# Optimization experiments

Measured on AMD Instinct MI355X. Metric: run time of the kernel, lower is better.

## Reference

```python
import jax, jax.numpy as jnp
import numpy as np

NUM_GROUPS = 32
EPS = 1e-5

def group_norm(x, gamma, beta):
    # x: [B, C, L]
    B, C, L = x.shape
    g = x.reshape(B, NUM_GROUPS, C // NUM_GROUPS, L)
    mu = g.mean(axis=(2, 3), keepdims=True)
    var = g.var(axis=(2, 3), keepdims=True)
    g = (g - mu) * jax.lax.rsqrt(var + EPS)
    h = g.reshape(B, C, L)
    return h * gamma[None, :, None] + beta[None, :, None]

def conv1x1(h, W, b):
    # h: [B, C, L], W: [Cout, Cin], b: [Cout] -> [B, Cout, L]
    return jnp.einsum('oc,bcl->bol', W, h) + b[None, :, None]

def setup_inputs() -> dict:
    key = jax.random.key(0)
    ks = jax.random.split(key, 10)
    B, C, L = 8, 512, 2048
    s = 1.0 / np.sqrt(C)
    inp = {
        'x': jax.random.normal(ks[0], (B, C, L), dtype=jnp.float32),
        'gn_gamma': jnp.ones((C,), jnp.float32),
        'gn_beta': jnp.zeros((C,), jnp.float32),
        'Wq': jax.random.normal(ks[1], (C, C), jnp.float32) * s,
        'bq': jnp.zeros((C,), jnp.float32),
        'Wk': jax.random.normal(ks[2], (C, C), jnp.float32) * s,
        'bk': jnp.zeros((C,), jnp.float32),
        'Wv': jax.random.normal(ks[3], (C, C), jnp.float32) * s,
        'bv': jnp.zeros((C,), jnp.float32),
        'Wo': jax.random.normal(ks[4], (C, C), jnp.float32) * s,
        'bo': jnp.zeros((C,), jnp.float32),
    }
    return inp

def reference(x, gn_gamma, gn_beta, Wq, bq, Wk, bk, Wv, bv, Wo, bo):
    B, C, L = x.shape
    h = group_norm(x, gn_gamma, gn_beta)
    q = conv1x1(h, Wq, bq)  # [B, C, L]
    k = conv1x1(h, Wk, bk)  # [B, C, L]
    v = conv1x1(h, Wv, bv)  # [B, C, L]
    scale = 1.0 / jnp.sqrt(jnp.float32(C)).astype(x.dtype)
    w = jnp.einsum('bci,bcj->bij', q, k) * scale  # [B, L, L]
    w = jax.nn.softmax(w, axis=-1)
    a = jnp.einsum('bij,bcj->bci', w, v)  # [B, C, L]
    return x + conv1x1(a, Wo, bo)
```

## Files before the change

### kernel.cpp

```cpp
#include <hip/hip_runtime.h>
#include <hip/hip_bf16.h>

#define B_ 8
#define C_ 512
#define L_ 2048
#define G_ 32

typedef __attribute__((ext_vector_type(8))) short bf16x8;
typedef __attribute__((ext_vector_type(4))) float f32x4;

__device__ __forceinline__ float b2f(short h) {
    union { unsigned u; float f; } c; c.u = ((unsigned)(unsigned short)h) << 16; return c.f;
}
__device__ __forceinline__ short f2b(float f) {
    union { float f; unsigned u; } c; c.f = f;
    unsigned r = (c.u + 0x7FFFu + ((c.u >> 16) & 1u)) >> 16;
    return (short)r;
}

__device__ __forceinline__ void load_lds16(const void* g, void* s) {
    __builtin_amdgcn_global_load_lds(
        (const __attribute__((address_space(1))) void*)g,
        (__attribute__((address_space(3))) void*)s, 16, 0, 0);
}

__global__ __launch_bounds__(256) void zero_f32(float* __restrict__ p) {
    p[(size_t)blockIdx.x * 256 + threadIdx.x] = 0.f;
}

__global__ __launch_bounds__(256) void cvt_w(
    const float* __restrict__ a, const float* __restrict__ b,
    const float* __restrict__ c, const float* __restrict__ d,
    short* __restrict__ o)
{
    const float* src = (blockIdx.y == 0) ? a : (blockIdx.y == 1) ? b
                     : (blockIdx.y == 2) ? c : d;
    short* dst = o + (size_t)blockIdx.y * (C_ * C_);
    int i = (blockIdx.x * 256 + threadIdx.x) * 4;
    float4 v = *(const float4*)(src + i);
    short4 r;
    r.x = f2b(v.x); r.y = f2b(v.y); r.z = f2b(v.z); r.w = f2b(v.w);
    *(short4*)(dst + i) = r;
}

__global__ __launch_bounds__(256) void groupnorm_tr(
    const float* __restrict__ x, const float* __restrict__ gamma,
    const float* __restrict__ beta, short* __restrict__ h_t)
{
    int bg = blockIdx.x;
    int b = bg >> 5, g = bg & 31;
    const float* xg = x + ((size_t)b * C_ + (size_t)g * 16) * L_;
    int t = threadIdx.x;
    float s = 0.f, ss = 0.f;
    for (int i = t; i < 8192; i += 256) {
        float4 v = ((const float4*)xg)[i];
        s  += v.x + v.y + v.z + v.w;
        ss += v.x * v.x + v.y * v.y + v.z * v.z + v.w * v.w;
    }
    #pragma unroll
    for (int o = 32; o > 0; o >>= 1) { s += __shfl_down(s, o); ss += __shfl_down(ss, o); }
    __shared__ float rs[4], rss[4], stats[2], gam[16], bet[16];
    int wave = t >> 6, lane = t & 63;
    if (lane == 0) { rs[wave] = s; rss[wave] = ss; }
    if (t < 16) { gam[t] = gamma[g * 16 + t]; bet[t] = beta[g * 16 + t]; }
    __syncthreads();
    if (t == 0) {
        float S = rs[0] + rs[1] + rs[2] + rs[3];
        float SS = rss[0] + rss[1] + rss[2] + rss[3];
        float mean = S * (1.f / 32768.f);
        float var = SS * (1.f / 32768.f) - mean * mean;
        stats[0] = mean; stats[1] = rsqrtf(var + 1e-5f);
    }
    __syncthreads();
    float mean = stats[0], rstd = stats[1];
    short* ho = h_t + (size_t)b * L_ * C_ + (size_t)g * 16;
    for (int i = t; i < 32768; i += 256) {
        int cl = i & 15, l = i >> 4;
        float xv = xg[cl * L_ + l];
        float hv = (xv - mean) * rstd * gam[cl] + bet[cl];
        ho[(size_t)l * C_ + cl] = f2b(hv);
    }
}

template<int BM, int BIAS_MODE, bool RESID, bool OUTF32, bool EXPSUM, bool ROWDIV>
__global__ __launch_bounds__(BM * 2) void gemm_bt(
    const short* __restrict__ A, const short* __restrict__ Bt,
    void* __restrict__ Co, const float* __restrict__ bias,
    const float* __restrict__ bias2, const float* __restrict__ resid,
    float* __restrict__ rowsum,
    int N, int K, int lda, int ldb, int ldc,
    long sA, long sB, long sC, float alpha)
{
    constexpr int T = BM * 2;
    constexpr int RPP = T / 8;
    __shared__ __align__(16) short As[BM * 64];
    __shared__ __align__(16) short Bs[128 * 64];

    int nbx = gridDim.x, nby = gridDim.y, nbz = gridDim.z;
    int lin = blockIdx.x + nbx * (blockIdx.y + nby * blockIdx.z);
    int total = nbx * nby * nbz;
    int bx, by, bz;
    if ((total & 7) == 0) {
        int chunk = total >> 3;
        int logical = (lin & 7) * chunk + (lin >> 3);
        bx = logical % nbx; int t2 = logical / nbx; by = t2 % nby; bz = t2 / nby;
    } else { bx = blockIdx.x; by = blockIdx.y; bz = blockIdx.z; }

    const short* Ab = A + (size_t)bz * sA;
    const short* Bb = Bt + (size_t)bz * sB;
    int m0 = by * BM, n0 = bx * 128;
    int t = threadIdx.x, lane = t & 63;
    int wave = t >> 6;
    int wm = wave >> 1, wn = wave & 1;

    f32x4 acc[4][4] = {};

    int rs_ = t >> 3, cs_ = t & 7;
    int gcol = ((cs_ ^ (rs_ & 7)) << 3);
    const short* gA = Ab + (size_t)(m0 + rs_) * lda + gcol;
    const short* gB = Bb + (size_t)(n0 + rs_) * ldb + gcol;
    int fr = lane & 15, fq = lane >> 4;
    int ch0 = (fq ^ (fr & 7)) << 3;
    int ch1 = ((4 | fq) ^ (fr & 7)) << 3;

    for (int k0 = 0; k0 < K; k0 += 64) {
        __syncthreads();
        #pragma unroll
        for (int i = 0; i < BM / RPP; i++)
            load_lds16(gA + (size_t)(RPP * i) * lda, As + i * (RPP * 64) + t * 8);
        #pragma unroll
        for (int i = 0; i < 128 / RPP; i++)
            load_lds16(gB + (size_t)(RPP * i) * ldb, Bs + i * (RPP * 64) + t * 8);
        gA += 64; gB += 64;
        __syncthreads();
        #pragma unroll
        for (int kk = 0; kk < 2; kk++) {
            int ch = kk ? ch1 : ch0;
            bf16x8 af[4], bfr[4];
            #pragma unroll
            for (int i = 0; i < 4; i++) {
                int R = wm * 64 + i * 16 + fr;
                af[i] = *(const bf16x8*)(As + R * 64 + ch);
            }
            #pragma unroll
            for (int j = 0; j < 4; j++) {
                int R = wn * 64 + j * 16 + fr;
                bfr[j] = *(const bf16x8*)(Bs + R * 64 + ch);
            }
            #pragma unroll
            for (int mt = 0; mt < 4; mt++)
                #pragma unroll
                for (int nt = 0; nt < 4; nt++)
                    acc[mt][nt] = __builtin_amdgcn_mfma_f32_16x16x32_bf16(
                        af[mt], bfr[nt], acc[mt][nt], 0, 0, 0);
        }
    }

    size_t cb = (size_t)bz * sC;
    int crow = (lane >> 4) * 4;
    int wrow = wm * 64;
    float psum[4][4];
    float inv[4][4];
    if (EXPSUM) {
        #pragma unroll
        for (int mt = 0; mt < 4; mt++)
            #pragma unroll
            for (int r = 0; r < 4; r++) psum[mt][r] = 0.f;
    }
    if (ROWDIV) {
        #pragma unroll
        for (int mt = 0; mt < 4; mt++)
            #pragma unroll
            for (int r = 0; r < 4; r++) {
                int m = m0 + wrow + mt * 16 + crow + r;
                inv[mt][r] = 1.f / rowsum[(size_t)bz * L_ + m];
            }
    }
    #pragma unroll
    for (int mt = 0; mt < 4; mt++) {
        #pragma unroll
        for (int nt = 0; nt < 4; nt++) {
            int n = n0 + wn * 64 + nt * 16 + fr;
            float bn = 0.f;
            if (BIAS_MODE == 3) bn = (n < 512) ? bias[n] : bias2[n - 512];
            #pragma unroll
            for (int r = 0; r < 4; r++) {
                int m = m0 + wrow + mt * 16 + crow + r;
                float v = acc[mt][nt][r] * alpha;
                if (EXPSUM) { v = __expf(v); psum[mt][r] += v; }
                if (ROWDIV) v *= inv[mt][r];
                if (BIAS_MODE == 3) v += bn;
                if (BIAS_MODE == 2) v += bias[m];
                size_t idx = cb + (size_t)m * ldc + n;
                if (RESID) v += resid[idx];
                if (OUTF32) ((float*)Co)[idx] = v;
                else        ((short*)Co)[idx] = f2b(v);
            }
        }
    }
    if (EXPSUM) {
        #pragma unroll
        for (int mt = 0; mt < 4; mt++)
            #pragma unroll
            for (int r = 0; r < 4; r++) {
                float s = psum[mt][r];
                s += __shfl_xor(s, 1); s += __shfl_xor(s, 2);
                s += __shfl_xor(s, 4); s += __shfl_xor(s, 8);
                if ((lane & 15) == 0) {
                    int m = m0 + wrow + mt * 16 + crow + r;
                    atomicAdd(rowsum + (size_t)bz * L_ + m, s);
                }
            }
    }
}

extern "C" void kernel_launch(void* const* d_in, const int* in_sizes, int n_in,
                              void* d_out, int out_size, void* d_ws, size_t ws_size,
                              hipStream_t stream)
{
    const float* x     = (const float*)d_in[0];
    const float* gamma = (const float*)d_in[1];
    const float* beta  = (const float*)d_in[2];
    const float* Wq    = (const float*)d_in[3];
    const float* bq    = (const float*)d_in[4];
    const float* Wk    = (const float*)d_in[5];
    const float* bk    = (const float*)d_in[6];
    const float* Wv    = (const float*)d_in[7];
    const float* bv    = (const float*)d_in[8];
    const float* Wo    = (const float*)d_in[9];
    const float* bo    = (const float*)d_in[10];
    float* out = (float*)d_out;

    const size_t MiB = 1024 * 1024;
    const size_t CC = (size_t)C_ * C_;
    const size_t LC = (size_t)L_ * C_;
    const size_t LL = (size_t)L_ * L_;
    const size_t wbytes = 4 * CC * sizeof(short);

    const size_t perb = 16 * MiB + L_ * sizeof(float);
    int nb = 1;
    for (int c = 8; c >= 1; c >>= 1)
        if (ws_size >= wbytes + (size_t)c * perb) { nb = c; break; }

    short* wq_b = (short*)d_ws;
    short* wv_b = wq_b + 2 * CC;
    short* wo_b = wv_b + CC;
    short* h_t  = wo_b + CC;
    short* qk_t = h_t + (size_t)nb * LC;
    short* v_   = qk_t + (size_t)nb * 2 * LC;
    short* S    = v_  + (size_t)nb * LC;
    float* rsum = (float*)(S + (size_t)nb * LL);
    short* a_t  = h_t;

    const long sLC = (long)LC;
    const long sLL = (long)LL;
    const float scale = 0.044194173824159216f;

    cvt_w<<<dim3(C_ * C_ / 1024, 4), 256, 0, stream>>>(Wq, Wk, Wv, Wo, wq_b);

    for (int b0 = 0; b0 < B_; b0 += nb) {
        const float* xb = x + (size_t)b0 * LC;
        float* outb = out + (size_t)b0 * LC;

        zero_f32<<<dim3(nb * L_ / 256), 256, 0, stream>>>(rsum);
        groupnorm_tr<<<dim3(nb * G_), 256, 0, stream>>>(xb, gamma, beta, h_t);

        gemm_bt<128, 3, false, false, false, false><<<dim3(8, 16, nb), 256, 0, stream>>>(
            h_t, wq_b, qk_t, bq, bk, nullptr, nullptr,
            1024, 512, 512, 512, 1024, sLC, 0, 2 * sLC, 1.f);
        gemm_bt<128, 2, false, false, false, false><<<dim3(16, 4, nb), 256, 0, stream>>>(
            wv_b, h_t, v_, bv, nullptr, nullptr, nullptr,
            2048, 512, 512, 512, 2048, 0, sLC, sLC, 1.f);
        gemm_bt<256, 0, false, false, true, false><<<dim3(16, 8, nb), 512, 0, stream>>>(
            qk_t, qk_t + 512, S, nullptr, nullptr, nullptr, rsum,
            2048, 512, 1024, 1024, 2048, 2 * sLC, 2 * sLC, sLL, scale);
        gemm_bt<128, 0, false, false, false, true><<<dim3(4, 16, nb), 256, 0, stream>>>(
            S, v_, a_t, nullptr, nullptr, nullptr, rsum,
            512, 2048, 2048, 2048, 512, sLL, sLC, sLC, 1.f);
        gemm_bt<128, 2, true, true, false, false><<<dim3(16, 4, nb), 256, 0, stream>>>(
            wo_b, a_t, outb, bo, nullptr, xb, nullptr,
            2048, 512, 512, 512, 2048, 0, sLC, sLC, 1.f);
    }
}
```

Before: 313.3 us.

## Replace LDS-staged GEMM with register double-buffered direct global fragment loads

Drops the shared-memory staging and barriers from the bf16 MFMA GEMM. Each wave now loads its A/B fragments directly from global memory into registers, with double buffering across k-steps. Tile shapes are retuned per call, including a wide 1x8-wave tile for the attention-times-V GEMM. This removes LDS traffic and synchronisation, but gives up cross-wave data reuse and relies on caches for repeated fragment reads.

```diff
diff --git a/kernel.cpp b/kernel.cpp
--- a/kernel.cpp
+++ b/kernel.cpp
@@ -16,12 +16,6 @@
     union { float f; unsigned u; } c; c.f = f;
     unsigned r = (c.u + 0x7FFFu + ((c.u >> 16) & 1u)) >> 16;
     return (short)r;
-}
-
-__device__ __forceinline__ void load_lds16(const void* g, void* s) {
-    __builtin_amdgcn_global_load_lds(
-        (const __attribute__((address_space(1))) void*)g,
-        (__attribute__((address_space(3))) void*)s, 16, 0, 0);
 }
 
 __global__ __launch_bounds__(256) void zero_f32(float* __restrict__ p) {
@@ -82,20 +76,15 @@
     }
 }
 
-template<int BM, int BIAS_MODE, bool RESID, bool OUTF32, bool EXPSUM, bool ROWDIV>
-__global__ __launch_bounds__(BM * 2) void gemm_bt(
+template<int WM, int WN, int NT, int NS, int BIAS_MODE, bool RESID, bool OUTF32,
+         bool EXPSUM, bool ROWDIV>
+__global__ __launch_bounds__(WM * WN * 64) void gemm_rf(
     const short* __restrict__ A, const short* __restrict__ Bt,
     void* __restrict__ Co, const float* __restrict__ bias,
     const float* __restrict__ bias2, const float* __restrict__ resid,
     float* __restrict__ rowsum,
-    int N, int K, int lda, int ldb, int ldc,
-    long sA, long sB, long sC, float alpha)
-{
-    constexpr int T = BM * 2;
-    constexpr int RPP = T / 8;
-    __shared__ __align__(16) short As[BM * 64];
-    __shared__ __align__(16) short Bs[128 * 64];
-
+    int lda, int ldb, int ldc, long sA, long sB, long sC, float alpha)
+{
     int nbx = gridDim.x, nby = gridDim.y, nbz = gridDim.z;
     int lin = blockIdx.x + nbx * (blockIdx.y + nby * blockIdx.z);
     int total = nbx * nby * nbz;
@@ -108,52 +97,46 @@
 
     const short* Ab = A + (size_t)bz * sA;
     const short* Bb = Bt + (size_t)bz * sB;
-    int m0 = by * BM, n0 = bx * 128;
+    int m0 = by * (WM * 64), n0 = bx * (WN * NT * 16);
     int t = threadIdx.x, lane = t & 63;
     int wave = t >> 6;
-    int wm = wave >> 1, wn = wave & 1;
-
-    f32x4 acc[4][4] = {};
-
-    int rs_ = t >> 3, cs_ = t & 7;
-    int gcol = ((cs_ ^ (rs_ & 7)) << 3);
-    const short* gA = Ab + (size_t)(m0 + rs_) * lda + gcol;
-    const short* gB = Bb + (size_t)(n0 + rs_) * ldb + gcol;
+    int wm = wave % WM, wn = wave / WM;
     int fr = lane & 15, fq = lane >> 4;
-    int ch0 = (fq ^ (fr & 7)) << 3;
-    int ch1 = ((4 | fq) ^ (fr & 7)) << 3;
-
-    for (int k0 = 0; k0 < K; k0 += 64) {
-        __syncthreads();
-        #pragma unroll
-        for (int i = 0; i < BM / RPP; i++)
-            load_lds16(gA + (size_t)(RPP * i) * lda, As + i * (RPP * 64) + t * 8);
-        #pragma unroll
-        for (int i = 0; i < 128 / RPP; i++)
-            load_lds16(gB + (size_t)(RPP * i) * ldb, Bs + i * (RPP * 64) + t * 8);
-        gA += 64; gB += 64;
-        __syncthreads();
-        #pragma unroll
-        for (int kk = 0; kk < 2; kk++) {
-            int ch = kk ? ch1 : ch0;
-            bf16x8 af[4], bfr[4];
-            #pragma unroll
-            for (int i = 0; i < 4; i++) {
-                int R = wm * 64 + i * 16 + fr;
-                af[i] = *(const bf16x8*)(As + R * 64 + ch);
-            }
-            #pragma unroll
-            for (int j = 0; j < 4; j++) {
-                int R = wn * 64 + j * 16 + fr;
-                bfr[j] = *(const bf16x8*)(Bs + R * 64 + ch);
-            }
+
+    const short* pA[4];
+    const short* pB[NT];
+    #pragma unroll
+    for (int mt = 0; mt < 4; mt++)
+        pA[mt] = Ab + (size_t)(m0 + wm * 64 + mt * 16 + fr) * lda + fq * 8;
+    #pragma unroll
+    for (int nt = 0; nt < NT; nt++)
+        pB[nt] = Bb + (size_t)(n0 + wn * (NT * 16) + nt * 16 + fr) * ldb + fq * 8;
+
+    f32x4 acc[4][NT] = {};
+    bf16x8 af[2][4], bg[2][NT];
+
+    #pragma unroll
+    for (int mt = 0; mt < 4; mt++) af[0][mt] = *(const bf16x8*)(pA[mt]);
+    #pragma unroll
+    for (int nt = 0; nt < NT; nt++) bg[0][nt] = *(const bf16x8*)(pB[nt]);
+
+    #pragma unroll 8
+    for (int s = 0; s < NS; s++) {
+        int p = s & 1;
+        if (s + 1 < NS) {
             #pragma unroll
             for (int mt = 0; mt < 4; mt++)
-                #pragma unroll
-                for (int nt = 0; nt < 4; nt++)
-                    acc[mt][nt] = __builtin_amdgcn_mfma_f32_16x16x32_bf16(
-                        af[mt], bfr[nt], acc[mt][nt], 0, 0, 0);
+                af[p ^ 1][mt] = *(const bf16x8*)(pA[mt] + (s + 1) * 32);
+            #pragma unroll
+            for (int nt = 0; nt < NT; nt++)
+                bg[p ^ 1][nt] = *(const bf16x8*)(pB[nt] + (s + 1) * 32);
         }
+        #pragma unroll
+        for (int mt = 0; mt < 4; mt++)
+            #pragma unroll
+            for (int nt = 0; nt < NT; nt++)
+                acc[mt][nt] = __builtin_amdgcn_mfma_f32_16x16x32_bf16(
+                    af[p][mt], bg[p][nt], acc[mt][nt], 0, 0, 0);
     }
 
     size_t cb = (size_t)bz * sC;
@@ -179,8 +162,8 @@
     #pragma unroll
     for (int mt = 0; mt < 4; mt++) {
         #pragma unroll
-        for (int nt = 0; nt < 4; nt++) {
-            int n = n0 + wn * 64 + nt * 16 + fr;
+        for (int nt = 0; nt < NT; nt++) {
+            int n = n0 + wn * (NT * 16) + nt * 16 + fr;
             float bn = 0.f;
             if (BIAS_MODE == 3) bn = (n < 512) ? bias[n] : bias2[n - 512];
             #pragma unroll
@@ -265,20 +248,25 @@
         zero_f32<<<dim3(nb * L_ / 256), 256, 0, stream>>>(rsum);
         groupnorm_tr<<<dim3(nb * G_), 256, 0, stream>>>(xb, gamma, beta, h_t);
 
-        gemm_bt<128, 3, false, false, false, false><<<dim3(8, 16, nb), 256, 0, stream>>>(
+        gemm_rf<2, 2, 4, 16, 3, false, false, false, false>
+            <<<dim3(8, 16, nb), 256, 0, stream>>>(
             h_t, wq_b, qk_t, bq, bk, nullptr, nullptr,
-            1024, 512, 512, 512, 1024, sLC, 0, 2 * sLC, 1.f);
-        gemm_bt<128, 2, false, false, false, false><<<dim3(16, 4, nb), 256, 0, stream>>>(
+            512, 512, 1024, sLC, 0, 2 * sLC, 1.f);
+        gemm_rf<2, 2, 4, 16, 2, false, false, false, false>
+            <<<dim3(16, 4, nb), 256, 0, stream>>>(
             wv_b, h_t, v_, bv, nullptr, nullptr, nullptr,
-            2048, 512, 512, 512, 2048, 0, sLC, sLC, 1.f);
-        gemm_bt<256, 0, false, false, true, false><<<dim3(16, 8, nb), 512, 0, stream>>>(
+            512, 512, 2048, 0, sLC, sLC, 1.f);
+        gemm_rf<2, 2, 4, 16, 0, false, false, true, false>
+            <<<dim3(16, 16, nb), 256, 0, stream>>>(
             qk_t, qk_t + 512, S, nullptr, nullptr, nullptr, rsum,
-            2048, 512, 1024, 1024, 2048, 2 * sLC, 2 * sLC, sLL, scale);
-        gemm_bt<128, 0, false, false, false, true><<<dim3(4, 16, nb), 256, 0, stream>>>(
+            1024, 1024, 2048, 2 * sLC, 2 * sLC, sLL, scale);
+        gemm_rf<1, 8, 4, 64, 0, false, false, false, true>
+            <<<dim3(1, 32, nb), 512, 0, stream>>>(
             S, v_, a_t, nullptr, nullptr, nullptr, rsum,
-            512, 2048, 2048, 2048, 512, sLL, sLC, sLC, 1.f);
-        gemm_bt<128, 2, true, true, false, false><<<dim3(16, 4, nb), 256, 0, stream>>>(
+            2048, 2048, 512, sLL, sLC, sLC, 1.f);
+        gemm_rf<2, 2, 4, 16, 2, true, true, false, false>
+            <<<dim3(16, 4, nb), 256, 0, stream>>>(
             wo_b, a_t, outb, bo, nullptr, xb, nullptr,
-            2048, 512, 512, 512, 2048, 0, sLC, sLC, 1.f);
-    }
-}
+            512, 512, 2048, 0, sLC, sLC, 1.f);
+    }
+}
```

After: 545.3 us. +74.1%, slower.
